# Kernel tuning notes

Hardware: AMD Instinct MI355X
Metric: run time of the kernel (lower is better)

## Reference

```python
import jax, jax.numpy as jnp
import numpy as np

B, T, C = 4, 2048, 1024
H = 16
DH = C // H


def setup_inputs() -> dict:
    key = jax.random.key(0)
    k1, k2, k3 = jax.random.split(key, 3)
    x = jax.random.normal(k1, (B, T, C), dtype=jnp.float32)
    w_qkv = jax.random.normal(k2, (3 * C, C), dtype=jnp.float32) * (1.0 / np.sqrt(C))
    w_out = jax.random.normal(k3, (C, C), dtype=jnp.float32) * (1.0 / np.sqrt(C))
    attn_mask = jnp.ones((B, T), dtype=jnp.int32)
    return {"x": x, "attn_mask": attn_mask, "w_qkv": w_qkv, "w_out": w_out}


def reference(x, attn_mask, w_qkv, w_out):
    b, t, c = x.shape
    h, dh = H, DH
    qkv = jnp.einsum('btc,fc->btf', x, w_qkv)  # [B,T,3C]
    q, k, v = jnp.split(qkv, 3, axis=-1)
    # [B,H,T,Dh]
    q = q.reshape(b, t, h, dh).transpose(0, 2, 1, 3)
    k = k.reshape(b, t, h, dh).transpose(0, 2, 1, 3)
    v = v.reshape(b, t, h, dh).transpose(0, 2, 1, 3)
    scale = jnp.sqrt(jnp.float32(dh))
    scores = jnp.einsum('bhqd,bhkd->bhqk', q, k) / scale  # [B,H,T,T]
    causal = jnp.tril(jnp.ones((t, t), dtype=bool))
    mask = causal[None, None, :, :] & (attn_mask[:, None, None, :] != 0)
    scores = jnp.where(mask, scores, -jnp.inf)
    p = jax.nn.softmax(scores, axis=-1)
    p = jnp.where(jnp.isnan(p), 0.0, p)  # nan_to_num for fully-masked rows
    out = jnp.einsum('bhqk,bhkd->bhqd', p, v)
    out = out.transpose(0, 2, 1, 3).reshape(b, t, c)
    return jnp.einsum('btc,fc->btf', out, w_out)
```

## Files before the change

kernel.cpp:

```cpp
#include <hip/hip_runtime.h>
#include <cstdint>
#include <cmath>


#define Bb 4
#define Tt 2048
#define Cc 1024
#define Hh 16
#define DHd 64
#define Mm (Bb*Tt)

typedef __attribute__((ext_vector_type(8))) short bf16x8;
typedef __attribute__((ext_vector_type(4))) short s16x4;
typedef __attribute__((ext_vector_type(4))) float f32x4;
typedef __attribute__((ext_vector_type(2))) unsigned int u32x2;

__device__ __forceinline__ short f2bf(float f) {
  uint32_t u = __builtin_bit_cast(uint32_t, f);
  u = (u + 0x7fffu + ((u >> 16) & 1u)) >> 16;
  return (short)(uint16_t)u;
}

__device__ __forceinline__ uint32_t cvtpk(float lo, float hi) {
  uint32_t r;
  asm("v_cvt_pk_bf16_f32 %0, %1, %2" : "=v"(r) : "v"(lo), "v"(hi));
  return r;
}

__device__ __forceinline__ f32x4 mfma16(s16x4 a, s16x4 b, f32x4 c) {
#if __has_builtin(__builtin_amdgcn_mfma_f32_16x16x16_bf16)
  return __builtin_amdgcn_mfma_f32_16x16x16_bf16(a, b, c, 0, 0, 0);
#elif __has_builtin(__builtin_amdgcn_mfma_f32_16x16x16bf16_1k)
  return __builtin_amdgcn_mfma_f32_16x16x16bf16_1k(a, b, c, 0, 0, 0);
#else
  f32x4 d;
  asm("v_mfma_f32_16x16x16_bf16 %0, %1, %2, %3" : "=v"(d) : "v"(a), "v"(b), "v"(c));
  return d;
#endif
}

__global__ void cvt_bf16(const float* __restrict__ in, short* __restrict__ out, int n4) {
  int i = blockIdx.x * blockDim.x + threadIdx.x;
  if (i >= n4) return;
  f32x4 v = reinterpret_cast<const f32x4*>(in)[i];
  s16x4 o;
  o.x = f2bf(v.x); o.y = f2bf(v.y); o.z = f2bf(v.z); o.w = f2bf(v.w);
  reinterpret_cast<s16x4*>(out)[i] = o;
}

#define BK 32

template<int MODE>
__global__ __launch_bounds__(256) void gemm_bt(
    const short* __restrict__ A, const short* __restrict__ Bt, int K, int N,
    float* __restrict__ Cout,
    short* __restrict__ qb, short* __restrict__ kb, short* __restrict__ vtb)
{
  __shared__ __align__(16) short As[128*BK];
  __shared__ __align__(16) short Bs[128*BK];
  const int tid = threadIdx.x;
  const int lane = tid & 63, wid = tid >> 6;
  const int wr = wid >> 1, wc = wid & 1;
  const int bm = blockIdx.y, bn = blockIdx.x;
  const int r16 = lane & 15, g = lane >> 4;

  f32x4 acc[4][4];
#pragma unroll
  for (int i = 0; i < 4; ++i)
#pragma unroll
    for (int j = 0; j < 4; ++j) acc[i][j] = (f32x4)0.0f;

  const int srow = lane >> 2;
  const int scol = (lane & 3) * 8;
  const int ch0 = wid * 2;

  const int nk = K / BK;
  for (int kt = 0; kt < nk; ++kt) {
    const int k0 = kt * BK;
#pragma unroll
    for (int c = 0; c < 2; ++c) {
      const int chunk = ch0 + c;
      const int row = chunk * 16 + srow;
      const short* ga = A  + (size_t)(bm*128 + row)*K + k0 + scol;
      const short* gb = Bt + (size_t)(bn*128 + row)*K + k0 + scol;
      __builtin_amdgcn_global_load_lds((const __attribute__((address_space(1))) void*)ga,
                                       (__attribute__((address_space(3))) void*)(&As[chunk*512]), 16, 0, 0);
      __builtin_amdgcn_global_load_lds((const __attribute__((address_space(1))) void*)gb,
                                       (__attribute__((address_space(3))) void*)(&Bs[chunk*512]), 16, 0, 0);
    }
    __syncthreads();

    bf16x8 af[4], bfv[4];
#pragma unroll
    for (int mi = 0; mi < 4; ++mi)
      af[mi] = *reinterpret_cast<const bf16x8*>(&As[(wr*64 + mi*16 + r16)*BK + g*8]);
#pragma unroll
    for (int ni = 0; ni < 4; ++ni)
      bfv[ni] = *reinterpret_cast<const bf16x8*>(&Bs[(wc*64 + ni*16 + r16)*BK + g*8]);
#pragma unroll
    for (int mi = 0; mi < 4; ++mi)
#pragma unroll
      for (int ni = 0; ni < 4; ++ni)
        acc[mi][ni] = __builtin_amdgcn_mfma_f32_16x16x32_bf16(af[mi], bfv[ni], acc[mi][ni], 0, 0, 0);
    __syncthreads();
  }

#pragma unroll
  for (int mi = 0; mi < 4; ++mi) {
    const int row0 = bm*128 + wr*64 + mi*16 + g*4;
#pragma unroll
    for (int ni = 0; ni < 4; ++ni) {
      const int col_g = bn*128 + wc*64 + ni*16 + r16;
      if (MODE == 1) {
#pragma unroll
        for (int r = 0; r < 4; ++r)
          Cout[(size_t)(row0 + r) * N + col_g] = acc[mi][ni][r];
      } else {
        const int which = col_g >> 10;
        const int hd = col_g & 1023;
        const int h = hd >> 6, d = hd & 63;
        const int b = row0 >> 11, t0 = row0 & 2047;
        const int bh = b*Hh + h;
        if (which == 0) {
#pragma unroll
          for (int r = 0; r < 4; ++r)
            qb[(((size_t)bh*Tt + t0 + r) << 6) + d] = f2bf(acc[mi][ni][r] * 0.18033688f);
        } else if (which == 1) {
#pragma unroll
          for (int r = 0; r < 4; ++r)
            kb[(((size_t)bh*Tt + t0 + r) << 6) + d] = f2bf(acc[mi][ni][r]);
        } else {
          u32x2 w;
          w.x = cvtpk(acc[mi][ni][0], acc[mi][ni][1]);
          w.y = cvtpk(acc[mi][ni][2], acc[mi][ni][3]);
          *reinterpret_cast<u32x2*>(vtb + ((size_t)bh*DHd + d)*Tt + t0) = w;
        }
      }
    }
  }
}

__global__ __launch_bounds__(256) void attn_fwd(
    const short* __restrict__ qbf, const short* __restrict__ kbf,
    const short* __restrict__ vtb, const int* __restrict__ am,
    short* __restrict__ ob)
{
  __shared__ __align__(16) short Ks[2][64*64];
  __shared__ __align__(16) short Vts[2][64*64];
  const int tid = threadIdx.x;
  const int lane = tid & 63, wid = tid >> 6;
  const int r16 = lane & 15, g = lane >> 4;

  const int lin = blockIdx.x;
  const int xcd = lin & 7;
  const int idx = lin >> 3;
  const int bh  = xcd * 8 + (idx & 7);
  const int qi_raw = idx >> 3;
  const int grp = qi_raw >> 2, rem = qi_raw & 3;
  const int qi = (grp == 0) ? 15 - rem : (grp == 1) ? rem : (grp == 2) ? 11 - rem : 4 + rem;
  const int b = bh >> 4, h = bh & 15;
  const int q0 = qi * 128;
  const int wq0 = q0 + wid * 32;

  const size_t kbase = (size_t)bh * Tt * DHd;
  const size_t vbase = (size_t)bh * DHd * Tt;

  const int srow0 = tid >> 3;
  const int p8    = tid & 7;
  const int ubase = tid & 448;

#define ASTAGE(SLOT, T0) do {                                                  \
    _Pragma("unroll")                                                          \
    for (int c_ = 0; c_ < 2; ++c_) {                                           \
      const int row_ = c_*32 + srow0;                                          \
      const int sp_  = (p8 ^ (row_ & 7)) * 8;                                  \
      const short* gk_ = kbf + kbase + (size_t)((T0) + row_)*DHd + sp_;        \
      const short* gv_ = vtb + vbase + (size_t)row_*Tt + (T0) + sp_;           \
      __builtin_amdgcn_global_load_lds(                                        \
          (const __attribute__((address_space(1))) void*)gk_,                  \
          (__attribute__((address_space(3))) void*)(&Ks[SLOT][(c_*256 + ubase)*8]), 16, 0, 0); \
      __builtin_amdgcn_global_load_lds(                                        \
          (const __attribute__((address_space(1))) void*)gv_,                  \
          (__attribute__((address_space(3))) void*)(&Vts[SLOT][(c_*256 + ubase)*8]), 16, 0, 0); \
    }                                                                          \
  } while (0)

  bf16x8 qf[2][2];
#pragma unroll
  for (int m = 0; m < 2; ++m) {
    const short* qbase = qbf + ((size_t)bh*Tt + wq0 + m*16 + r16)*DHd;
    qf[m][0] = *reinterpret_cast<const bf16x8*>(qbase + g*8);
    qf[m][1] = *reinterpret_cast<const bf16x8*>(qbase + 32 + g*8);
  }

  f32x4 o[2][4];
  float mrow[2], lrow[2];
#pragma unroll
  for (int m = 0; m < 2; ++m) {
    mrow[m] = -INFINITY; lrow[m] = 0.f;
#pragma unroll
    for (int i = 0; i < 4; ++i) o[m][i] = (f32x4)0.0f;
  }

  const int nkv = 2*qi + 2;
  int amv = am[b*Tt + lane];

  ASTAGE(0, 0);
  __syncthreads();

  for (int kv = 0; kv < nkv; ++kv) {
    const int cur = kv & 1;
    const int kv0 = kv * 64;
    const unsigned long long mb = __ballot(amv != 0);
    int amv_next = 0;
    if (kv + 1 < nkv) {
      ASTAGE(cur ^ 1, kv0 + 64);
      amv_next = am[b*Tt + kv0 + 64 + lane];
    }

    if (kv0 <= wq0 + 31) {
      const char* kbp = (const char*)Ks[cur];
      const char* vbp = (const char*)Vts[cur];
      const int swzr = (r16 & 7) << 4;

      f32x4 st[2][4];
      __builtin_amdgcn_s_setprio(1);
#pragma unroll
      for (int kt = 0; kt < 4; ++kt) {
        const int rb = (kt*16 + r16)*128;
        const bf16x8 ka0 = *reinterpret_cast<const bf16x8*>(kbp + ((rb + g*16) ^ swzr));
        const bf16x8 ka1 = *reinterpret_cast<const bf16x8*>(kbp + ((rb + 64 + g*16) ^ swzr));
#pragma unroll
        for (int m = 0; m < 2; ++m) {
          f32x4 t = (f32x4)0.0f;
          t = __builtin_amdgcn_mfma_f32_16x16x32_bf16(ka0, qf[m][0], t, 0, 0, 0);
          t = __builtin_amdgcn_mfma_f32_16x16x32_bf16(ka1, qf[m][1], t, 0, 0, 0);
          st[m][kt] = t;
        }
      }
      __builtin_amdgcn_s_setprio(0);

      const bool notall = (mb != ~0ull);
      const bool diag = (kv0 + 63 > wq0);
      if (diag || notall) {
#pragma unroll
        for (int m = 0; m < 2; ++m) {
          const int qrow = wq0 + m*16 + r16;
#pragma unroll
          for (int kt = 0; kt < 4; ++kt)
#pragma unroll
            for (int r = 0; r < 4; ++r) {
              const int kl = kt*16 + g*4 + r;
              bool ok = !diag || (kv0 + kl <= qrow);
              if (notall) ok = ok && ((mb >> kl) & 1ull);
              if (!ok) st[m][kt][r] = -3.0e38f;
            }
        }
      }

      float mx[2];
#pragma unroll
      for (int m = 0; m < 2; ++m) {
        f32x4 t0, t1;
#pragma unroll
        for (int i = 0; i < 4; ++i) { t0[i] = fmaxf(st[m][0][i], st[m][1][i]); t1[i] = fmaxf(st[m][2][i], st[m][3][i]); }
#pragma unroll
        for (int i = 0; i < 4; ++i) t0[i] = fmaxf(t0[i], t1[i]);
        mx[m] = fmaxf(fmaxf(t0[0], t0[1]), fmaxf(t0[2], t0[3]));
      }
      {
        float a0 = __shfl_xor(mx[0], 16), a1 = __shfl_xor(mx[1], 16);
        mx[0] = fmaxf(mx[0], a0); mx[1] = fmaxf(mx[1], a1);
        a0 = __shfl_xor(mx[0], 32); a1 = __shfl_xor(mx[1], 32);
        mx[0] = fmaxf(mx[0], a0); mx[1] = fmaxf(mx[1], a1);
      }
      const bool need = __any((mx[0] > mrow[0] + 8.f) || (mx[1] > mrow[1] + 8.f));
      if (need) {
#pragma unroll
        for (int m = 0; m < 2; ++m) {
          const float mnew = fmaxf(mrow[m], mx[m]);
          const float alpha = __builtin_amdgcn_exp2f(mrow[m] - mnew);
          mrow[m] = mnew;
          lrow[m] *= alpha;
#pragma unroll
          for (int dt = 0; dt < 4; ++dt) o[m][dt] *= alpha;
        }
      }

      s16x4 pb[2][4];
      float rsum[2];
#pragma unroll
      for (int m = 0; m < 2; ++m) {
#pragma unroll
        for (int kt = 0; kt < 4; ++kt)
#pragma unroll
          for (int r = 0; r < 4; ++r)
            st[m][kt][r] = __builtin_amdgcn_exp2f(st[m][kt][r] - mrow[m]);
#pragma unroll
        for (int kt = 0; kt < 4; ++kt) {
          u32x2 w;
          w.x = cvtpk(st[m][kt][0], st[m][kt][1]);
          w.y = cvtpk(st[m][kt][2], st[m][kt][3]);
          pb[m][kt] = __builtin_bit_cast(s16x4, w);
        }
        f32x4 s4;
#pragma unroll
        for (int i = 0; i < 4; ++i) s4[i] = st[m][0][i] + st[m][1][i] + st[m][2][i] + st[m][3][i];
        rsum[m] = (s4[0] + s4[1]) + (s4[2] + s4[3]);
      }
      {
        float a0 = __shfl_xor(rsum[0], 16), a1 = __shfl_xor(rsum[1], 16);
        rsum[0] += a0; rsum[1] += a1;
        a0 = __shfl_xor(rsum[0], 32); a1 = __shfl_xor(rsum[1], 32);
        rsum[0] += a0; rsum[1] += a1;
      }
      lrow[0] += rsum[0]; lrow[1] += rsum[1];

      __builtin_amdgcn_s_setprio(1);
#pragma unroll
      for (int dt = 0; dt < 4; ++dt) {
        const int row = dt*16 + r16;
        const int rb = row*128;
        const int r7 = row & 7;
#pragma unroll
        for (int kt = 0; kt < 4; ++kt) {
          const s16x4 va = *reinterpret_cast<const s16x4*>(
              vbp + rb + ((((kt<<1) + (g>>1)) ^ r7) << 4) + (g & 1)*8);
          o[0][dt] = mfma16(va, pb[0][kt], o[0][dt]);
          o[1][dt] = mfma16(va, pb[1][kt], o[1][dt]);
        }
      }
      __builtin_amdgcn_s_setprio(0);
    }

    amv = amv_next;
    __syncthreads();
  }

#pragma unroll
  for (int m = 0; m < 2; ++m) {
    const float inv = (mrow[m] > -1e37f) ? 1.0f / lrow[m] : 0.f;
    short* obase = ob + ((size_t)(b*Tt + wq0 + m*16 + r16))*Cc + h*DHd;
#pragma unroll
    for (int dt = 0; dt < 4; ++dt) {
      u32x2 w;
      w.x = cvtpk(o[m][dt][0]*inv, o[m][dt][1]*inv);
      w.y = cvtpk(o[m][dt][2]*inv, o[m][dt][3]*inv);
      *reinterpret_cast<u32x2*>(obase + dt*16 + g*4) = w;
    }
  }
#undef ASTAGE
}

extern "C" void kernel_launch(void* const* d_in, const int* in_sizes, int n_in,
                              void* d_out, int out_size, void* d_ws, size_t ws_size,
                              hipStream_t stream) {
  const float* x    = (const float*)d_in[0];
  const int*   am   = (const int*)d_in[1];
  const float* wqkv = (const float*)d_in[2];
  const float* wout = (const float*)d_in[3];
  float* out = (float*)d_out;

  const size_t mc = (size_t)Mm * Cc;
  short* ws    = (short*)d_ws;
  short* xb    = ws;
  short* wqkvb = xb + mc;
  short* woutb = wqkvb + (size_t)3*Cc*Cc;
  short* qbuf  = woutb + (size_t)Cc*Cc;
  short* kbuf  = qbuf + mc;
  short* vtbuf = kbuf + mc;
  short* attnb = xb;

  cvt_bf16<<<(int)((mc/4 + 255)/256), 256, 0, stream>>>(x, xb, (int)(mc/4));
  cvt_bf16<<<(3*Cc*Cc/4 + 255)/256, 256, 0, stream>>>(wqkv, wqkvb, 3*Cc*Cc/4);
  cvt_bf16<<<(Cc*Cc/4 + 255)/256, 256, 0, stream>>>(wout, woutb, Cc*Cc/4);

  gemm_bt<0><<<dim3(3*Cc/128, Mm/128), 256, 0, stream>>>(
      xb, wqkvb, Cc, 3*Cc, nullptr, qbuf, kbuf, vtbuf);

  attn_fwd<<<dim3(Bb*Hh*Tt/128), 256, 0, stream>>>(qbuf, kbuf, vtbuf, am, attnb);

  gemm_bt<1><<<dim3(Cc/128, Mm/128), 256, 0, stream>>>(
      attnb, woutb, Cc, Cc, out, nullptr, nullptr, nullptr);
}
```

Measured before the change: 219.4 us.

## Pair causal attention tiles per block for balanced work with 64-row Q tiles

The attention kernel now launches 1024 blocks, each processing two 64-row query tiles in sequence (tile 31-p then tile p), so every block does the same total number of KV iterations under the causal mask. Each wave handles 16 query rows instead of 32, which halves its accumulator and score registers. The trade-offs are that each K/V tile loaded into LDS is reused by fewer query rows, so total K/V traffic roughly doubles, and the two phases run serially inside a block.

After: 228.8 us. +4.3%, slower.

```diff
diff --git a/kernel.cpp b/kernel.cpp
--- a/kernel.cpp
+++ b/kernel.cpp
@@ -153,14 +153,10 @@
 
   const int lin = blockIdx.x;
   const int xcd = lin & 7;
-  const int idx = lin >> 3;
-  const int bh  = xcd * 8 + (idx & 7);
-  const int qi_raw = idx >> 3;
-  const int grp = qi_raw >> 2, rem = qi_raw & 3;
-  const int qi = (grp == 0) ? 15 - rem : (grp == 1) ? rem : (grp == 2) ? 11 - rem : 4 + rem;
+  const int rest = lin >> 3;
+  const int bh  = xcd * 8 + (rest & 7);
+  const int p   = rest >> 3;
   const int b = bh >> 4, h = bh & 15;
-  const int q0 = qi * 128;
-  const int wq0 = q0 + wid * 32;
 
   const size_t kbase = (size_t)bh * Tt * DHd;
   const size_t vbase = (size_t)bh * DHd * Tt;
@@ -185,136 +181,111 @@
     }                                                                          \
   } while (0)
 
-  bf16x8 qf[2][2];
-#pragma unroll
-  for (int m = 0; m < 2; ++m) {
-    const short* qbase = qbf + ((size_t)bh*Tt + wq0 + m*16 + r16)*DHd;
-    qf[m][0] = *reinterpret_cast<const bf16x8*>(qbase + g*8);
-    qf[m][1] = *reinterpret_cast<const bf16x8*>(qbase + 32 + g*8);
-  }
-
-  f32x4 o[2][4];
-  float mrow[2], lrow[2];
-#pragma unroll
-  for (int m = 0; m < 2; ++m) {
-    mrow[m] = -INFINITY; lrow[m] = 0.f;
-#pragma unroll
-    for (int i = 0; i < 4; ++i) o[m][i] = (f32x4)0.0f;
-  }
-
-  const int nkv = 2*qi + 2;
-  int amv = am[b*Tt + lane];
-
-  ASTAGE(0, 0);
-  __syncthreads();
-
-  for (int kv = 0; kv < nkv; ++kv) {
-    const int cur = kv & 1;
-    const int kv0 = kv * 64;
-    const unsigned long long mb = __ballot(amv != 0);
-    int amv_next = 0;
-    if (kv + 1 < nkv) {
-      ASTAGE(cur ^ 1, kv0 + 64);
-      amv_next = am[b*Tt + kv0 + 64 + lane];
-    }
-
-    if (kv0 <= wq0 + 31) {
+#pragma unroll 1
+  for (int ph = 0; ph < 2; ++ph) {
+    const int item = (ph == 0) ? 31 - p : p;
+    const int wq0 = item*64 + wid*16;
+    const int nkv = item + 1;
+
+    const short* qbase = qbf + ((size_t)bh*Tt + wq0 + r16)*DHd;
+    const bf16x8 qf0 = *reinterpret_cast<const bf16x8*>(qbase + g*8);
+    const bf16x8 qf1 = *reinterpret_cast<const bf16x8*>(qbase + 32 + g*8);
+
+    f32x4 o[4];
+    float mrow = -INFINITY, lrow = 0.f;
+#pragma unroll
+    for (int i = 0; i < 4; ++i) o[i] = (f32x4)0.0f;
+
+    int amv = am[b*Tt + lane];
+    ASTAGE(0, 0);
+    __syncthreads();
+
+#pragma unroll 1
+    for (int kv = 0; kv < nkv; ++kv) {
+      const int cur = kv & 1;
+      const int kv0 = kv * 64;
+      const unsigned long long mb = __ballot(amv != 0);
+      int amv_next = 0;
+      if (kv + 1 < nkv) {
+        ASTAGE(cur ^ 1, kv0 + 64);
+        amv_next = am[b*Tt + kv0 + 64 + lane];
+      }
+
       const char* kbp = (const char*)Ks[cur];
       const char* vbp = (const char*)Vts[cur];
       const int swzr = (r16 & 7) << 4;
 
-      f32x4 st[2][4];
+      f32x4 st[4];
       __builtin_amdgcn_s_setprio(1);
 #pragma unroll
       for (int kt = 0; kt < 4; ++kt) {
         const int rb = (kt*16 + r16)*128;
         const bf16x8 ka0 = *reinterpret_cast<const bf16x8*>(kbp + ((rb + g*16) ^ swzr));
         const bf16x8 ka1 = *reinterpret_cast<const bf16x8*>(kbp + ((rb + 64 + g*16) ^ swzr));
-#pragma unroll
-        for (int m = 0; m < 2; ++m) {
-          f32x4 t = (f32x4)0.0f;
-          t = __builtin_amdgcn_mfma_f32_16x16x32_bf16(ka0, qf[m][0], t, 0, 0, 0);
-          t = __builtin_amdgcn_mfma_f32_16x16x32_bf16(ka1, qf[m][1], t, 0, 0, 0);
-          st[m][kt] = t;
-        }
+        f32x4 t = (f32x4)0.0f;
+        t = __builtin_amdgcn_mfma_f32_16x16x32_bf16(ka0, qf0, t, 0, 0, 0);
+        t = __builtin_amdgcn_mfma_f32_16x16x32_bf16(ka1, qf1, t, 0, 0, 0);
+        st[kt] = t;
       }
       __builtin_amdgcn_s_setprio(0);
 
       const bool notall = (mb != ~0ull);
       const bool diag = (kv0 + 63 > wq0);
       if (diag || notall) {
-#pragma unroll
-        for (int m = 0; m < 2; ++m) {
-          const int qrow = wq0 + m*16 + r16;
-#pragma unroll
-          for (int kt = 0; kt < 4; ++kt)
-#pragma unroll
-            for (int r = 0; r < 4; ++r) {
-              const int kl = kt*16 + g*4 + r;
-              bool ok = !diag || (kv0 + kl <= qrow);
-              if (notall) ok = ok && ((mb >> kl) & 1ull);
-              if (!ok) st[m][kt][r] = -3.0e38f;
-            }
-        }
-      }
-
-      float mx[2];
-#pragma unroll
-      for (int m = 0; m < 2; ++m) {
+        const int qrow = wq0 + r16;
+#pragma unroll
+        for (int kt = 0; kt < 4; ++kt)
+#pragma unroll
+          for (int r = 0; r < 4; ++r) {
+            const int kl = kt*16 + g*4 + r;
+            bool ok = !diag || (kv0 + kl <= qrow);
+            if (notall) ok = ok && ((mb >> kl) & 1ull);
+            if (!ok) st[kt][r] = -3.0e38f;
+          }
+      }
+
+      float mx;
+      {
         f32x4 t0, t1;
 #pragma unroll
-        for (int i = 0; i < 4; ++i) { t0[i] = fmaxf(st[m][0][i], st[m][1][i]); t1[i] = fmaxf(st[m][2][i], st[m][3][i]); }
+        for (int i = 0; i < 4; ++i) { t0[i] = fmaxf(st[0][i], st[1][i]); t1[i] = fmaxf(st[2][i], st[3][i]); }
 #pragma unroll
         for (int i = 0; i < 4; ++i) t0[i] = fmaxf(t0[i], t1[i]);
-        mx[m] = fmaxf(fmaxf(t0[0], t0[1]), fmaxf(t0[2], t0[3]));
+        mx = fmaxf(fmaxf(t0[0], t0[1]), fmaxf(t0[2], t0[3]));
+        mx = fmaxf(mx, __shfl_xor(mx, 16));
+        mx = fmaxf(mx, __shfl_xor(mx, 32));
+      }
+      if (__any(mx > mrow + 8.f)) {
+        const float mnew = fmaxf(mrow, mx);
+        const float alpha = __builtin_amdgcn_exp2f(mrow - mnew);
+        mrow = mnew;
+        lrow *= alpha;
+#pragma unroll
+        for (int dt = 0; dt < 4; ++dt) o[dt] *= alpha;
+      }
+
+      s16x4 pb[4];
+#pragma unroll
+      for (int kt = 0; kt < 4; ++kt)
+#pragma unroll
+        for (int r = 0; r < 4; ++r)
+          st[kt][r] = __builtin_amdgcn_exp2f(st[kt][r] - mrow);
+#pragma unroll
+      for (int kt = 0; kt < 4; ++kt) {
+        u32x2 w;
+        w.x = cvtpk(st[kt][0], st[kt][1]);
+        w.y = cvtpk(st[kt][2], st[kt][3]);
+        pb[kt] = __builtin_bit_cast(s16x4, w);
       }
       {
-        float a0 = __shfl_xor(mx[0], 16), a1 = __shfl_xor(mx[1], 16);
-        mx[0] = fmaxf(mx[0], a0); mx[1] = fmaxf(mx[1], a1);
-        a0 = __shfl_xor(mx[0], 32); a1 = __shfl_xor(mx[1], 32);
-        mx[0] = fmaxf(mx[0], a0); mx[1] = fmaxf(mx[1], a1);
-      }
-      const bool need = __any((mx[0] > mrow[0] + 8.f) || (mx[1] > mrow[1] + 8.f));
-      if (need) {
-#pragma unroll
-        for (int m = 0; m < 2; ++m) {
-          const float mnew = fmaxf(mrow[m], mx[m]);
-          const float alpha = __builtin_amdgcn_exp2f(mrow[m] - mnew);
-          mrow[m] = mnew;
-          lrow[m] *= alpha;
-#pragma unroll
-          for (int dt = 0; dt < 4; ++dt) o[m][dt] *= alpha;
-        }
-      }
-
-      s16x4 pb[2][4];
-      float rsum[2];
-#pragma unroll
-      for (int m = 0; m < 2; ++m) {
-#pragma unroll
-        for (int kt = 0; kt < 4; ++kt)
-#pragma unroll
-          for (int r = 0; r < 4; ++r)
-            st[m][kt][r] = __builtin_amdgcn_exp2f(st[m][kt][r] - mrow[m]);
-#pragma unroll
-        for (int kt = 0; kt < 4; ++kt) {
-          u32x2 w;
-          w.x = cvtpk(st[m][kt][0], st[m][kt][1]);
-          w.y = cvtpk(st[m][kt][2], st[m][kt][3]);
-          pb[m][kt] = __builtin_bit_cast(s16x4, w);
-        }
         f32x4 s4;
 #pragma unroll
-        for (int i = 0; i < 4; ++i) s4[i] = st[m][0][i] + st[m][1][i] + st[m][2][i] + st[m][3][i];
-        rsum[m] = (s4[0] + s4[1]) + (s4[2] + s4[3]);
-      }
-      {
-        float a0 = __shfl_xor(rsum[0], 16), a1 = __shfl_xor(rsum[1], 16);
-        rsum[0] += a0; rsum[1] += a1;
-        a0 = __shfl_xor(rsum[0], 32); a1 = __shfl_xor(rsum[1], 32);
-        rsum[0] += a0; rsum[1] += a1;
-      }
-      lrow[0] += rsum[0]; lrow[1] += rsum[1];
+        for (int i = 0; i < 4; ++i) s4[i] = st[0][i] + st[1][i] + st[2][i] + st[3][i];
+        float rsum = (s4[0] + s4[1]) + (s4[2] + s4[3]);
+        rsum += __shfl_xor(rsum, 16);
+        rsum += __shfl_xor(rsum, 32);
+        lrow += rsum;
+      }
 
       __builtin_amdgcn_s_setprio(1);
 #pragma unroll
@@ -326,26 +297,22 @@
         for (int kt = 0; kt < 4; ++kt) {
           const s16x4 va = *reinterpret_cast<const s16x4*>(
               vbp + rb + ((((kt<<1) + (g>>1)) ^ r7) << 4) + (g & 1)*8);
-          o[0][dt] = mfma16(va, pb[0][kt], o[0][dt]);
-          o[1][dt] = mfma16(va, pb[1][kt], o[1][dt]);
+          o[dt] = mfma16(va, pb[kt], o[dt]);
         }
       }
       __builtin_amdgcn_s_setprio(0);
+
+      amv = amv_next;
+      __syncthreads();
     }
 
-    amv = amv_next;
-    __syncthreads();
-  }
-
-#pragma unroll
-  for (int m = 0; m < 2; ++m) {
-    const float inv = (mrow[m] > -1e37f) ? 1.0f / lrow[m] : 0.f;
-    short* obase = ob + ((size_t)(b*Tt + wq0 + m*16 + r16))*Cc + h*DHd;
+    const float inv = (mrow > -1e37f) ? 1.0f / lrow : 0.f;
+    short* obase = ob + ((size_t)(b*Tt + wq0 + r16))*Cc + h*DHd;
 #pragma unroll
     for (int dt = 0; dt < 4; ++dt) {
       u32x2 w;
-      w.x = cvtpk(o[m][dt][0]*inv, o[m][dt][1]*inv);
-      w.y = cvtpk(o[m][dt][2]*inv, o[m][dt][3]*inv);
+      w.x = cvtpk(o[dt][0]*inv, o[dt][1]*inv);
+      w.y = cvtpk(o[dt][2]*inv, o[dt][3]*inv);
       *reinterpret_cast<u32x2*>(obase + dt*16 + g*4) = w;
     }
   }
@@ -378,7 +345,7 @@
   gemm_bt<0><<<dim3(3*Cc/128, Mm/128), 256, 0, stream>>>(
       xb, wqkvb, Cc, 3*Cc, nullptr, qbuf, kbuf, vtbuf);
 
-  attn_fwd<<<dim3(Bb*Hh*Tt/128), 256, 0, stream>>>(qbuf, kbuf, vtbuf, am, attnb);
+  attn_fwd<<<dim3(1024), 256, 0, stream>>>(qbuf, kbuf, vtbuf, am, attnb);
 
   gemm_bt<1><<<dim3(Cc/128, Mm/128), 256, 0, stream>>>(
       attnb, woutb, Cc, Cc, out, nullptr, nullptr, nullptr);
```
